# Kernel tuning notes

Measured on AMD Instinct MI355X. Metric: run time of the kernel, lower is better.

## Reference

```python
import jax, jax.numpy as jnp
import numpy as np

B, D, K, A = 32768, 256, 1024, 32
MIN_LOG_STD, MAX_LOG_STD = -20.0, 2.0


def setup_inputs() -> dict:
    key = jax.random.key(0)
    ks = jax.random.split(key, 9)
    return {
        "obs": jax.random.normal(ks[0], (B, D), dtype=jnp.float32),
        "mean_C": jax.random.normal(ks[1], (K, D), dtype=jnp.float32),
        "mean_sigma": jnp.abs(jax.random.normal(ks[2], (K,), dtype=jnp.float32)) + 0.1,
        "mean_w": jax.random.normal(ks[3], (A, K), dtype=jnp.float32),
        "mean_b": jax.random.normal(ks[4], (A,), dtype=jnp.float32),
        "std_C": jax.random.normal(ks[5], (K, D), dtype=jnp.float32),
        "std_sigma": jnp.abs(jax.random.normal(ks[6], (K,), dtype=jnp.float32)) + 0.1,
        "std_w": jax.random.normal(ks[7], (A, K), dtype=jnp.float32),
        "std_b": jax.random.normal(ks[8], (A,), dtype=jnp.float32),
    }


def _rbf(x, C, sigma_sq, w, b):
    # r[b,k] = sum_d (x[b,d] - C[k,d])^2, expanded to avoid a [B,K,D] intermediate
    x2 = jnp.sum(x * x, axis=-1, keepdims=True)           # [B,1]
    c2 = jnp.sum(C * C, axis=-1)[None, :]                  # [1,K]
    r = x2 - 2.0 * (x @ C.T) + c2                          # [B,K]
    phi = jnp.exp(-r / (2.0 * jnp.abs(sigma_sq)[None, :]))  # [B,K]
    return phi @ w.T + b[None, :]                          # [B,A]


def reference(obs, mean_C, mean_sigma, mean_w, mean_b,
              std_C, std_sigma, std_w, std_b):
    action_mean = _rbf(obs, mean_C, mean_sigma, mean_w, mean_b)
    std_raw = _rbf(obs, std_C, std_sigma, std_w, std_b)
    action_std = jnp.exp(jnp.clip(std_raw, MIN_LOG_STD, MAX_LOG_STD))
    return jnp.concatenate((action_mean, action_std), axis=-1)  # [B, 2A]
```

## Files before the change

### kernel.cpp

```cpp
#include <hip/hip_runtime.h>


typedef float floatx4 __attribute__((ext_vector_type(4)));
typedef int   intx4  __attribute__((ext_vector_type(4)));
typedef unsigned int u32;
typedef unsigned char u8;

constexpr float LOG2E = 1.4426950408889634f;
constexpr float QS    = 25.4f;
constexpr float SINV2 = (5.0f / 127.0f) * (5.0f / 127.0f);

__device__ __forceinline__ u32 pk_fp8(float a, float b, float c, float d) {
  u32 v = __builtin_amdgcn_cvt_pk_fp8_f32(a, b, 0u, 0);
  v = __builtin_amdgcn_cvt_pk_fp8_f32(c, d, v, 1);
  return v;
}
__device__ __forceinline__ long mk64(u32 lo, u32 hi) {
  return (long)lo | ((long)hi << 32);
}
__device__ __forceinline__ int q8(float x) {
  return (int)rintf(fminf(fmaxf(x * QS, -127.f), 127.f));
}
__device__ __forceinline__ u32 pk_i8(int a, int b, int c, int d) {
  return (u32)(a & 255) | ((u32)(b & 255) << 8) | ((u32)(c & 255) << 16) | ((u32)(d & 255) << 24);
}

__global__ void prep(const float* __restrict__ mC, const float* __restrict__ mS,
                     const float* __restrict__ sC, const float* __restrict__ sS,
                     const float* __restrict__ mw, const float* __restrict__ sw,
                     u8* __restrict__ Cb2, float* __restrict__ a2g,
                     float* __restrict__ g2n, u8* __restrict__ wb)
{
  const int blk = blockIdx.x;
  if (blk < 512) {
    const int wq = threadIdx.x >> 6;
    const int t  = threadIdx.x & 63;
    const int b  = blk * 4 + wq;
    const int half = b >> 10;
    const int k = b & 1023;
    const float* src = (half ? sC : mC) + (size_t)k * 256;
    float4 f = *(const float4*)(src + t * 4);
    int i0 = q8(f.x), i1 = q8(f.y), i2 = q8(f.z), i3 = q8(f.w);
    const int ct = b >> 6, row = b & 63;
    const int wvv = row >> 4, cc = row & 15;
    const int ks = t >> 4, qq = (t >> 2) & 3, j0 = (t & 3) * 4;
    *(u32*)(Cb2 + (size_t)ct * 16384 + wvv * 4096 + (16 * qq + cc) * 64 + 16 * ks + j0) =
        pk_i8(i0, i1, i2, i3);
    int is = i0 * i0 + i1 * i1 + i2 * i2 + i3 * i3;
    for (int off = 32; off > 0; off >>= 1) is += __shfl_down(is, off, 64);
    if (t == 0) {
      float sig = fabsf((half ? sS : mS)[k]);
      float t2 = SINV2 * LOG2E * 0.5f / sig;
      a2g[b] = 2.f * t2;
      g2n[b] = -t2 * (float)is;
    }
  } else {
    int i0 = (blk - 512) * 1024 + threadIdx.x * 4;
    int half = i0 >> 15;
    int rem  = i0 & 32767;
    const float* src = half ? sw : mw;
    float4 f = *(const float4*)(src + rem);
    ((u32*)wb)[i0 >> 2] = pk_fp8(f.x, f.y, f.z, f.w);
  }
}

__global__ __launch_bounds__(256, 2)
void policy_main(const float* __restrict__ obs,
                 const u8* __restrict__ Cb2,
                 const float* __restrict__ a2g,
                 const float* __restrict__ g2n,
                 const u8* __restrict__ wb,
                 const float* __restrict__ mbias,
                 const float* __restrict__ sbias,
                 float* __restrict__ out)
{
  __shared__ __align__(16) char smem[69888];
  float* x2p = (float*)(smem + 16384);
  float* red = (float*)smem;

  const int tid  = threadIdx.x;
  const int lane = tid & 63;
  const int wv   = tid >> 6;
  const int c    = lane & 15;
  const int q    = lane >> 4;
  const int row0 = blockIdx.x * 64;
  const int kslc = 16 * wv + 4 * q;
  const int cfo  = tid * 64;

#define LOADCF(CF, t)                                                     \
  { const u8* g0_ = Cb2 + (size_t)(t) * 16384 + cfo;                      \
    CF[0] = *(const intx4*)(g0_);                                         \
    CF[1] = *(const intx4*)(g0_ + 16);                                    \
    CF[2] = *(const intx4*)(g0_ + 32);                                    \
    CF[3] = *(const intx4*)(g0_ + 48); }

  intx4 cfU[4], cfV[4];
  LOADCF(cfU, 0)
  LOADCF(cfV, 1)

  #pragma unroll
  for (int i = 0; i < 4; ++i) {
    int s = i * 256 + tid;
    int row = s >> 4;
    int s16 = s & 15;
    int l16 = s16 ^ (row & 15);
    const float* src = obs + (size_t)(row0 + row) * 256 + l16 * 16;
    float4 f0 = ((const float4*)src)[0];
    float4 f1 = ((const float4*)src)[1];
    float4 f2 = ((const float4*)src)[2];
    float4 f3 = ((const float4*)src)[3];
    int a0 = q8(f0.x), a1v = q8(f0.y), a2v = q8(f0.z), a3 = q8(f0.w);
    int b0 = q8(f1.x), b1 = q8(f1.y), b2 = q8(f1.z), b3 = q8(f1.w);
    int c0 = q8(f2.x), c1 = q8(f2.y), c2 = q8(f2.z), c3 = q8(f2.w);
    int d0 = q8(f3.x), d1 = q8(f3.y), d2 = q8(f3.z), d3 = q8(f3.w);
    uint4 pk;
    pk.x = pk_i8(a0, a1v, a2v, a3);
    pk.y = pk_i8(b0, b1, b2, b3);
    pk.z = pk_i8(c0, c1, c2, c3);
    pk.w = pk_i8(d0, d1, d2, d3);
    *(uint4*)(smem + s * 16) = pk;
    int is = a0*a0 + a1v*a1v + a2v*a2v + a3*a3
           + b0*b0 + b1*b1 + b2*b2 + b3*b3
           + c0*c0 + c1*c1 + c2*c2 + c3*c3
           + d0*d0 + d1*d1 + d2*d2 + d3*d3;
    x2p[row * 16 + s16] = (float)is;
  }
  __syncthreads();

  intx4 ob[4][4];
  #pragma unroll
  for (int nt = 0; nt < 4; ++nt) {
    const int row = nt * 16 + c;
    #pragma unroll
    for (int ks = 0; ks < 4; ++ks) {
      int slot = (4 * ks + q) ^ (row & 15);
      ob[nt][ks] = *(const intx4*)(smem + row * 256 + slot * 16);
    }
  }
  if (tid < 64) {
    float s = 0.f;
    #pragma unroll
    for (int j = 0; j < 16; j += 4) {
      float4 a = *(const float4*)(x2p + tid * 16 + j);
      s += a.x + a.y + a.z + a.w;
    }
    x2p[1024 + tid] = s;
  }
  __syncthreads();

  float hx2[4];
  #pragma unroll
  for (int nt = 0; nt < 4; ++nt) hx2[nt] = 0.5f * x2p[1024 + nt * 16 + c];

  const intx4 Z4i = {0, 0, 0, 0};
  const floatx4 Z4 = {0.f, 0.f, 0.f, 0.f};
  floatx4 acc2m[2][4], acc2s[2][4];
  #pragma unroll
  for (int a2i = 0; a2i < 2; ++a2i)
    #pragma unroll
    for (int nt = 0; nt < 4; ++nt) {
      acc2m[a2i][nt] = Z4;
      acc2s[a2i][nt] = Z4;
    }

  intx4 a1A[4], a1B[4];
  float4 acA, gcA, acB, gcB;
  u32 pE[4], pc[4];

#define GEMM1T(CF, A1)                                                          \
  { A1[0] = __builtin_amdgcn_mfma_i32_16x16x64_i8(CF[0], ob[0][0], Z4i, 0, 0, 0); \
    A1[1] = __builtin_amdgcn_mfma_i32_16x16x64_i8(CF[0], ob[1][0], Z4i, 0, 0, 0); \
    A1[2] = __builtin_amdgcn_mfma_i32_16x16x64_i8(CF[0], ob[2][0], Z4i, 0, 0, 0); \
    A1[3] = __builtin_amdgcn_mfma_i32_16x16x64_i8(CF[0], ob[3][0], Z4i, 0, 0, 0); \
    _Pragma("unroll")                                                           \
    for (int ks = 1; ks < 4; ++ks) {                                            \
      A1[0] = __builtin_amdgcn_mfma_i32_16x16x64_i8(CF[ks], ob[0][ks], A1[0], 0, 0, 0); \
      A1[1] = __builtin_amdgcn_mfma_i32_16x16x64_i8(CF[ks], ob[1][ks], A1[1], 0, 0, 0); \
      A1[2] = __builtin_amdgcn_mfma_i32_16x16x64_i8(CF[ks], ob[2][ks], A1[2], 0, 0, 0); \
      A1[3] = __builtin_amdgcn_mfma_i32_16x16x64_i8(CF[ks], ob[3][ks], A1[3], 0, 0, 0); \
    } }

#define EXPP(A1, AC, GC, DST)                                                   \
  { _Pragma("unroll")                                                           \
    for (int nt = 0; nt < 4; ++nt) {                                            \
      float t0 = (float)A1[nt][0] - hx2[nt], t1 = (float)A1[nt][1] - hx2[nt];   \
      float t2 = (float)A1[nt][2] - hx2[nt], t3 = (float)A1[nt][3] - hx2[nt];   \
      DST[nt] = pk_fp8(__builtin_amdgcn_exp2f(fmaf(AC.x, t0, GC.x)),            \
                       __builtin_amdgcn_exp2f(fmaf(AC.y, t1, GC.y)),            \
                       __builtin_amdgcn_exp2f(fmaf(AC.z, t2, GC.z)),            \
                       __builtin_amdgcn_exp2f(fmaf(AC.w, t3, GC.w))); } }

#define GEMM2P(ACC, W0L, W0H, W1L, W1H)                                         \
  { long wA0 = mk64(W0L, W0H), wA1 = mk64(W1L, W1H);                            \
    _Pragma("unroll")                                                           \
    for (int nt = 0; nt < 4; ++nt) {                                            \
      long pb = mk64(pE[nt], pc[nt]);                                           \
      ACC[0][nt] = __builtin_amdgcn_mfma_f32_16x16x32_fp8_fp8(wA0, pb, ACC[0][nt], 0, 0, 0); \
      ACC[1][nt] = __builtin_amdgcn_mfma_f32_16x16x32_fp8_fp8(wA1, pb, ACC[1][nt], 0, 0, 0); \
    } }

  acA = *(const float4*)(a2g + kslc);
  gcA = *(const float4*)(g2n + kslc);
  GEMM1T(cfU, a1A)
  LOADCF(cfU, 2)

#define STEP(m, ACC, HB, DO_U)                                                  \
  {                                                                             \
    const int e = 2 * (m);                                                      \
    const int kbE = (e & 15) * 64 + kslc;                                       \
    const u8* wr0 = wb + (size_t)((HB) + c) * 1024 + kbE;                       \
    const u8* wr1 = wb + (size_t)((HB) + 16 + c) * 1024 + kbE;                  \
    u32 w0lo = *(const u32*)wr0, w0hi = *(const u32*)(wr0 + 64);                \
    u32 w1lo = *(const u32*)wr1, w1hi = *(const u32*)(wr1 + 64);                \
    acB = *(const float4*)(a2g + (e + 1) * 64 + kslc);                          \
    gcB = *(const float4*)(g2n + (e + 1) * 64 + kslc);                          \
    GEMM1T(cfV, a1B)                                                            \
    LOADCF(cfV, e + 3)                                                          \
    EXPP(a1A, acA, gcA, pE)                                                     \
    acA = *(const float4*)(a2g + (e + 2) * 64 + kslc);                          \
    gcA = *(const float4*)(g2n + (e + 2) * 64 + kslc);                          \
    GEMM1T(cfU, a1A)                                                            \
    if (DO_U) LOADCF(cfU, e + 4)                                                \
    EXPP(a1B, acB, gcB, pc)                                                     \
    GEMM2P(ACC, w0lo, w0hi, w1lo, w1hi)                                         \
  }

  #pragma unroll
  for (int m = 0; m < 8; ++m) STEP(m, acc2m, 0, 1)
  #pragma unroll
  for (int m = 8; m < 14; ++m) STEP(m, acc2s, 32, 1)
  STEP(14, acc2s, 32, 0)
  {
    const int kbE = (30 & 15) * 64 + kslc;
    const u8* wr0 = wb + (size_t)(32 + c) * 1024 + kbE;
    const u8* wr1 = wb + (size_t)(48 + c) * 1024 + kbE;
    u32 w0lo = *(const u32*)wr0, w0hi = *(const u32*)(wr0 + 64);
    u32 w1lo = *(const u32*)wr1, w1hi = *(const u32*)(wr1 + 64);
    acB = *(const float4*)(a2g + 31 * 64 + kslc);
    gcB = *(const float4*)(g2n + 31 * 64 + kslc);
    GEMM1T(cfV, a1B)
    EXPP(a1A, acA, gcA, pE)
    EXPP(a1B, acB, gcB, pc)
    GEMM2P(acc2s, w0lo, w0hi, w1lo, w1hi)
  }
#undef STEP
#undef GEMM1T
#undef EXPP
#undef GEMM2P
#undef LOADCF

  {
    float* myr = red + wv * 4352;
    #pragma unroll
    for (int a2i = 0; a2i < 2; ++a2i)
      #pragma unroll
      for (int nt = 0; nt < 4; ++nt) {
        *(floatx4*)(myr + (nt * 16 + c) * 68 + a2i * 16 + 4 * q)      = acc2m[a2i][nt];
        *(floatx4*)(myr + (nt * 16 + c) * 68 + 32 + a2i * 16 + 4 * q) = acc2s[a2i][nt];
      }
  }
  __syncthreads();

  #pragma unroll
  for (int i = 0; i < 16; ++i) {
    int idx = tid + 256 * i;
    int a = idx & 63;
    int b = idx >> 6;
    float v = red[b * 68 + a] + red[4352 + b * 68 + a] +
              red[8704 + b * 68 + a] + red[13056 + b * 68 + a];
    if (a < 32) {
      v += mbias[a];
    } else {
      v += sbias[a - 32];
      v = fminf(fmaxf(v, -20.f), 2.f);
      v = __builtin_amdgcn_exp2f(v * LOG2E);
    }
    out[(size_t)(row0 + b) * 64 + a] = v;
  }
}

extern "C" void kernel_launch(void* const* d_in, const int* in_sizes, int n_in,
                              void* d_out, int out_size, void* d_ws, size_t ws_size,
                              hipStream_t stream) {
  const float* obs = (const float*)d_in[0];
  const float* mC  = (const float*)d_in[1];
  const float* mS  = (const float*)d_in[2];
  const float* mW  = (const float*)d_in[3];
  const float* mB  = (const float*)d_in[4];
  const float* sC  = (const float*)d_in[5];
  const float* sS  = (const float*)d_in[6];
  const float* sW  = (const float*)d_in[7];
  const float* sB  = (const float*)d_in[8];
  float* out = (float*)d_out;

  u8*    Cb2 = (u8*)d_ws;
  float* a2g = (float*)((char*)d_ws + 2048 * 256);
  float* g2n = a2g + 2048;
  u8*    wb  = (u8*)(g2n + 2048);

  prep<<<576, 256, 0, stream>>>(mC, mS, sC, sS, mW, sW, Cb2, a2g, g2n, wb);
  policy_main<<<512, 256, 0, stream>>>(obs, Cb2, a2g, g2n, wb, mB, sB, out);
}
```

Baseline: 129.2 us.

## Pre-tile fp8 weights and centers into per-lane coalesced layouts

The prep kernel now writes the second-GEMM fp8 weights in a per-step, per-thread tiled order, so each step in the main kernel fetches its four weight dwords with one 16-byte load instead of four scattered 4-byte loads. The int8 center tiles are also relaid so that consecutive lanes read consecutive 16-byte chunks, which makes the LOADCF loads coalesced across the wavefront. The prep grid shrinks to match the new weight packing. The aim is to cut global-load instruction count and uncoalesced traffic in the hot loop, at the cost of a more intricate prep indexing scheme.

```diff
diff --git a/kernel.cpp b/kernel.cpp
--- a/kernel.cpp
+++ b/kernel.cpp
@@ -29,7 +29,7 @@
                      const float* __restrict__ sC, const float* __restrict__ sS,
                      const float* __restrict__ mw, const float* __restrict__ sw,
                      u8* __restrict__ Cb2, float* __restrict__ a2g,
-                     float* __restrict__ g2n, u8* __restrict__ wb)
+                     float* __restrict__ g2n, u8* __restrict__ wt)
 {
   const int blk = blockIdx.x;
   if (blk < 512) {
@@ -44,7 +44,7 @@
     const int ct = b >> 6, row = b & 63;
     const int wvv = row >> 4, cc = row & 15;
     const int ks = t >> 4, qq = (t >> 2) & 3, j0 = (t & 3) * 4;
-    *(u32*)(Cb2 + (size_t)ct * 16384 + wvv * 4096 + (16 * qq + cc) * 64 + 16 * ks + j0) =
+    *(u32*)(Cb2 + (size_t)ct * 16384 + wvv * 4096 + (ks * 64 + qq * 16 + cc) * 16 + j0) =
         pk_i8(i0, i1, i2, i3);
     int is = i0 * i0 + i1 * i1 + i2 * i2 + i3 * i3;
     for (int off = 32; off > 0; off >>= 1) is += __shfl_down(is, off, 64);
@@ -55,12 +55,24 @@
       g2n[b] = -t2 * (float)is;
     }
   } else {
-    int i0 = (blk - 512) * 1024 + threadIdx.x * 4;
-    int half = i0 >> 15;
-    int rem  = i0 & 32767;
-    const float* src = half ? sw : mw;
-    float4 f = *(const float4*)(src + rem);
-    ((u32*)wb)[i0 >> 2] = pk_fp8(f.x, f.y, f.z, f.w);
+    const int m   = blk - 512;
+    const int tid = threadIdx.x;
+    const int wv  = tid >> 6;
+    const int lane = tid & 63;
+    const int c   = lane & 15;
+    const int q   = lane >> 4;
+    const int kbE = ((2 * m) & 15) * 64 + 16 * wv + 4 * q;
+    const float* src = (m < 8) ? mw : sw;
+    float4 f00 = *(const float4*)(src + (size_t)c * 1024 + kbE);
+    float4 f01 = *(const float4*)(src + (size_t)c * 1024 + kbE + 64);
+    float4 f10 = *(const float4*)(src + (size_t)(16 + c) * 1024 + kbE);
+    float4 f11 = *(const float4*)(src + (size_t)(16 + c) * 1024 + kbE + 64);
+    uint4 o;
+    o.x = pk_fp8(f00.x, f00.y, f00.z, f00.w);
+    o.y = pk_fp8(f01.x, f01.y, f01.z, f01.w);
+    o.z = pk_fp8(f10.x, f10.y, f10.z, f10.w);
+    o.w = pk_fp8(f11.x, f11.y, f11.z, f11.w);
+    *(uint4*)(wt + ((size_t)m * 256 + tid) * 16) = o;
   }
 }
 
@@ -69,7 +81,7 @@
                  const u8* __restrict__ Cb2,
                  const float* __restrict__ a2g,
                  const float* __restrict__ g2n,
-                 const u8* __restrict__ wb,
+                 const u8* __restrict__ wt,
                  const float* __restrict__ mbias,
                  const float* __restrict__ sbias,
                  float* __restrict__ out)
@@ -85,14 +97,15 @@
   const int q    = lane >> 4;
   const int row0 = blockIdx.x * 64;
   const int kslc = 16 * wv + 4 * q;
-  const int cfo  = tid * 64;
+  const int cfo  = wv * 4096 + lane * 16;
+  const u8* wtl  = wt + (size_t)tid * 16;
 
 #define LOADCF(CF, t)                                                     \
   { const u8* g0_ = Cb2 + (size_t)(t) * 16384 + cfo;                      \
     CF[0] = *(const intx4*)(g0_);                                         \
-    CF[1] = *(const intx4*)(g0_ + 16);                                    \
-    CF[2] = *(const intx4*)(g0_ + 32);                                    \
-    CF[3] = *(const intx4*)(g0_ + 48); }
+    CF[1] = *(const intx4*)(g0_ + 1024);                                  \
+    CF[2] = *(const intx4*)(g0_ + 2048);                                  \
+    CF[3] = *(const intx4*)(g0_ + 3072); }
 
   intx4 cfU[4], cfV[4];
   LOADCF(cfU, 0)
@@ -190,8 +203,8 @@
                        __builtin_amdgcn_exp2f(fmaf(AC.z, t2, GC.z)),            \
                        __builtin_amdgcn_exp2f(fmaf(AC.w, t3, GC.w))); } }
 
-#define GEMM2P(ACC, W0L, W0H, W1L, W1H)                                         \
-  { long wA0 = mk64(W0L, W0H), wA1 = mk64(W1L, W1H);                            \
+#define GEMM2P(ACC, WV4)                                                        \
+  { long wA0 = mk64(WV4.x, WV4.y), wA1 = mk64(WV4.z, WV4.w);                    \
     _Pragma("unroll")                                                           \
     for (int nt = 0; nt < 4; ++nt) {                                            \
       long pb = mk64(pE[nt], pc[nt]);                                           \
@@ -204,14 +217,10 @@
   GEMM1T(cfU, a1A)
   LOADCF(cfU, 2)
 
-#define STEP(m, ACC, HB, DO_U)                                                  \
+#define STEP(m, ACC, DO_U)                                                      \
   {                                                                             \
     const int e = 2 * (m);                                                      \
-    const int kbE = (e & 15) * 64 + kslc;                                       \
-    const u8* wr0 = wb + (size_t)((HB) + c) * 1024 + kbE;                       \
-    const u8* wr1 = wb + (size_t)((HB) + 16 + c) * 1024 + kbE;                  \
-    u32 w0lo = *(const u32*)wr0, w0hi = *(const u32*)(wr0 + 64);                \
-    u32 w1lo = *(const u32*)wr1, w1hi = *(const u32*)(wr1 + 64);                \
+    uint4 wv4 = *(const uint4*)(wtl + (size_t)(m) * 4096);                      \
     acB = *(const float4*)(a2g + (e + 1) * 64 + kslc);                          \
     gcB = *(const float4*)(g2n + (e + 1) * 64 + kslc);                          \
     GEMM1T(cfV, a1B)                                                            \
@@ -222,26 +231,22 @@
     GEMM1T(cfU, a1A)                                                            \
     if (DO_U) LOADCF(cfU, e + 4)                                                \
     EXPP(a1B, acB, gcB, pc)                                                     \
-    GEMM2P(ACC, w0lo, w0hi, w1lo, w1hi)                                         \
-  }
-
-  #pragma unroll
-  for (int m = 0; m < 8; ++m) STEP(m, acc2m, 0, 1)
-  #pragma unroll
-  for (int m = 8; m < 14; ++m) STEP(m, acc2s, 32, 1)
-  STEP(14, acc2s, 32, 0)
+    GEMM2P(ACC, wv4)                                                            \
+  }
+
+  #pragma unroll
+  for (int m = 0; m < 8; ++m) STEP(m, acc2m, 1)
+  #pragma unroll
+  for (int m = 8; m < 14; ++m) STEP(m, acc2s, 1)
+  STEP(14, acc2s, 0)
   {
-    const int kbE = (30 & 15) * 64 + kslc;
-    const u8* wr0 = wb + (size_t)(32 + c) * 1024 + kbE;
-    const u8* wr1 = wb + (size_t)(48 + c) * 1024 + kbE;
-    u32 w0lo = *(const u32*)wr0, w0hi = *(const u32*)(wr0 + 64);
-    u32 w1lo = *(const u32*)wr1, w1hi = *(const u32*)(wr1 + 64);
+    uint4 wv4 = *(const uint4*)(wtl + (size_t)15 * 4096);
     acB = *(const float4*)(a2g + 31 * 64 + kslc);
     gcB = *(const float4*)(g2n + 31 * 64 + kslc);
     GEMM1T(cfV, a1B)
     EXPP(a1A, acA, gcA, pE)
     EXPP(a1B, acB, gcB, pc)
-    GEMM2P(acc2s, w0lo, w0hi, w1lo, w1hi)
+    GEMM2P(acc2s, wv4)
   }
 #undef STEP
 #undef GEMM1T
@@ -296,8 +301,8 @@
   u8*    Cb2 = (u8*)d_ws;
   float* a2g = (float*)((char*)d_ws + 2048 * 256);
   float* g2n = a2g + 2048;
-  u8*    wb  = (u8*)(g2n + 2048);
-
-  prep<<<576, 256, 0, stream>>>(mC, mS, sC, sS, mW, sW, Cb2, a2g, g2n, wb);
-  policy_main<<<512, 256, 0, stream>>>(obs, Cb2, a2g, g2n, wb, mB, sB, out);
-}
+  u8*    wt  = (u8*)(g2n + 2048);
+
+  prep<<<528, 256, 0, stream>>>(mC, mS, sC, sS, mW, sW, Cb2, a2g, g2n, wt);
+  policy_main<<<512, 256, 0, stream>>>(obs, Cb2, a2g, g2n, wt, mB, sB, out);
+}
```

Measured after the change: 117.1 us. 1.1x faster.
